# Optimization experiments

Hardware: AMD Instinct MI355X
Metric: run time of the kernel (lower is better)

Reference implementation:

```python
import jax, jax.numpy as jnp
import numpy as np

F = 256  # features
B, N = 16, 2048


def setup_inputs() -> dict:
    key = jax.random.key(0)
    ks = jax.random.split(key, 12)
    s = 1.0 / np.sqrt(F)
    return {
        "x": jax.random.normal(ks[0], (B, N, F), dtype=jnp.float32),
        "p": jax.random.normal(ks[1], (B, N, 3), dtype=jnp.float32),
        # nn.Linear weights: [out, in], y = x @ W.T + b
        "Wq": jax.random.normal(ks[2], (F, F), dtype=jnp.float32) * s,
        "bq": jax.random.normal(ks[3], (F,), dtype=jnp.float32) * s,
        "Wk": jax.random.normal(ks[4], (F, F), dtype=jnp.float32) * s,
        "bk": jax.random.normal(ks[5], (F,), dtype=jnp.float32) * s,
        "Wv": jax.random.normal(ks[6], (F, F), dtype=jnp.float32) * s,
        "bv": jax.random.normal(ks[7], (F,), dtype=jnp.float32) * s,
        # Conv1d kernel_size=1 == pointwise linear: W1 [F,3], W2 [F,F]
        "W1": jax.random.normal(ks[8], (F, 3), dtype=jnp.float32) * (1.0 / np.sqrt(3.0)),
        "b1": jax.random.normal(ks[9], (F,), dtype=jnp.float32) * (1.0 / np.sqrt(3.0)),
        "W2": jax.random.normal(ks[10], (F, F), dtype=jnp.float32) * s,
        "b2": jax.random.normal(ks[11], (F,), dtype=jnp.float32) * s,
    }


def reference(x, p, Wq, bq, Wk, bk, Wv, bv, W1, b1, W2, b2):
    # Positional encoder: Conv1d(3->F, k=1) + ReLU + Conv1d(F->F, k=1)
    pos = jnp.maximum(p @ W1.T + b1, 0.0) @ W2.T + b2  # [B, N, F]
    h = x + pos
    # NOTE: the original code swaps names: x_query = self.key(x), x_key = self.query(x)
    q = h @ Wk.T + bk  # x_query
    k = h @ Wq.T + bq  # x_key
    v = h @ Wv.T + bv  # x_value
    scale = 1.0 / np.sqrt(float(F))
    scores = jnp.einsum("bnf,bmf->bnm", q, k) * scale  # [B, N, N]
    attn = jax.nn.softmax(scores, axis=-1)
    return jnp.einsum("bnm,bmf->bnf", attn, v)  # [B, N, F]
```

## Files before the change

kernel.cpp:

```cpp
#include <hip/hip_runtime.h>

#define FEAT 256
#define SEQ  2048
#define NBATCH 16

typedef float  f32x4  __attribute__((ext_vector_type(4)));
typedef __bf16 bf16x8 __attribute__((ext_vector_type(8)));

__device__ __forceinline__ unsigned short f2bf(float f) {
  union { float f; unsigned int u; } v; v.f = f;
  unsigned int r = (v.u + 0x7fffu + ((v.u >> 16) & 1u)) >> 16;
  return (unsigned short)r;
}
__device__ __forceinline__ float bf2f(unsigned short u) {
  union { unsigned int u; float f; } v; v.u = ((unsigned int)u) << 16;
  return v.f;
}
__device__ __forceinline__ unsigned int pack2bf(float a, float b) {
  return (unsigned int)f2bf(a) | ((unsigned int)f2bf(b) << 16);
}

__device__ __forceinline__ float redsum16(float t) {
  t += __shfl_xor(t, 1);
  t += __shfl_xor(t, 2);
  t += __shfl_xor(t, 4);
  t += __shfl_xor(t, 8);
  return t;
}

__global__ __launch_bounds__(256) void k_wcvt(
    const float* __restrict__ Wq, const float* __restrict__ Wk,
    const float* __restrict__ Wv, const float* __restrict__ W2,
    unsigned short* __restrict__ Wqb, unsigned short* __restrict__ Wkb,
    unsigned short* __restrict__ Wvb, unsigned short* __restrict__ W2b) {
  int i = blockIdx.x * 256 + threadIdx.x;
  Wqb[i] = f2bf(Wq[i]);
  Wkb[i] = f2bf(Wk[i]);
  Wvb[i] = f2bf(Wv[i]);
  W2b[i] = f2bf(W2[i]);
}

__global__ __launch_bounds__(256) void k_pos_h(
    const float* __restrict__ x, const float* __restrict__ p,
    const float* __restrict__ W1, const float* __restrict__ b1,
    const unsigned short* __restrict__ W2b, const float* __restrict__ b2,
    unsigned short* __restrict__ hb) {
  __shared__ __align__(16) unsigned short tlds[64 * 264];
  __shared__ float pl[192];
  const int tid = threadIdx.x;
  const int blk = blockIdx.x;
  const int tok0 = blk * 64;
  if (tid < 192) pl[tid] = p[tok0 * 3 + tid];
  __syncthreads();
  const int j = tid;
  const float w0 = W1[j * 3 + 0], w1 = W1[j * 3 + 1], w2 = W1[j * 3 + 2];
  const float bb = b1[j];
#pragma unroll 4
  for (int tl = 0; tl < 64; ++tl) {
    float v = bb + pl[tl * 3 + 0] * w0 + pl[tl * 3 + 1] * w1 + pl[tl * 3 + 2] * w2;
    v = v > 0.f ? v : 0.f;
    tlds[tl * 264 + j] = f2bf(v);
  }
  __syncthreads();
  const int w = tid >> 6, lane = tid & 63;
  const int col = lane & 15, quad = lane >> 4;
  bf16x8 af[8];
  const unsigned short* arow = tlds + (w * 16 + col) * 264 + quad * 8;
#pragma unroll
  for (int ks = 0; ks < 8; ++ks) af[ks] = *(const bf16x8*)(arow + ks * 32);
#pragma unroll 1
  for (int ct = 0; ct < 16; ++ct) {
    f32x4 acc = {0.f, 0.f, 0.f, 0.f};
    const unsigned short* brow = W2b + (ct * 16 + col) * 256 + quad * 8;
#pragma unroll
    for (int ks = 0; ks < 8; ++ks) {
      bf16x8 bf = *(const bf16x8*)(brow + ks * 32);
      acc = __builtin_amdgcn_mfma_f32_16x16x32_bf16(af[ks], bf, acc, 0, 0, 0);
    }
    const int f = ct * 16 + col;
    const float bias = b2[f];
#pragma unroll
    for (int r = 0; r < 4; ++r) {
      const int tok = tok0 + w * 16 + quad * 4 + r;
      float v = acc[r] + bias + x[tok * 256 + f];
      hb[tok * 256 + f] = f2bf(v);
    }
  }
}

__global__ __launch_bounds__(256) void k_qkv(
    const unsigned short* __restrict__ hb,
    const unsigned short* __restrict__ Wqb, const float* __restrict__ bq,
    const unsigned short* __restrict__ Wkb, const float* __restrict__ bk,
    const unsigned short* __restrict__ Wvb, const float* __restrict__ bv,
    unsigned short* __restrict__ qb, unsigned short* __restrict__ kb,
    unsigned short* __restrict__ vtb) {
  const int tid = threadIdx.x, blk = blockIdx.x;
  const int ct0 = blockIdx.y * 8;
  const int w = tid >> 6, lane = tid & 63;
  const int col = lane & 15, quad = lane >> 4;
  const int row0 = blk * 128 + w * 32;
  bf16x8 af0[8], af1[8];
  const unsigned short* arow0 = hb + (size_t)(row0 + col) * 256 + quad * 8;
  const unsigned short* arow1 = arow0 + 16 * 256;
#pragma unroll
  for (int ks = 0; ks < 8; ++ks) {
    af0[ks] = *(const bf16x8*)(arow0 + ks * 32);
    af1[ks] = *(const bf16x8*)(arow1 + ks * 32);
  }
#pragma unroll 1
  for (int mat = 0; mat < 3; ++mat) {
    const unsigned short* W = (mat == 0) ? Wkb : ((mat == 1) ? Wqb : Wvb);
    const float* bias = (mat == 0) ? bk : ((mat == 1) ? bq : bv);
#pragma unroll 1
    for (int ct = ct0; ct < ct0 + 8; ++ct) {
      f32x4 a0 = {0.f, 0.f, 0.f, 0.f}, a1 = {0.f, 0.f, 0.f, 0.f};
      const unsigned short* brow = W + (ct * 16 + col) * 256 + quad * 8;
#pragma unroll
      for (int ks = 0; ks < 8; ++ks) {
        bf16x8 bf = *(const bf16x8*)(brow + ks * 32);
        a0 = __builtin_amdgcn_mfma_f32_16x16x32_bf16(af0[ks], bf, a0, 0, 0, 0);
        a1 = __builtin_amdgcn_mfma_f32_16x16x32_bf16(af1[ks], bf, a1, 0, 0, 0);
      }
      const int f = ct * 16 + col;
      const float bs = bias[f];
      if (mat < 2) {
        unsigned short* dst = (mat == 0) ? qb : kb;
#pragma unroll
        for (int r = 0; r < 4; ++r) {
          dst[(size_t)(row0 + quad * 4 + r) * 256 + f] = f2bf(a0[r] + bs);
          dst[(size_t)(row0 + 16 + quad * 4 + r) * 256 + f] = f2bf(a1[r] + bs);
        }
      } else {
        uint4 pk;
        pk.x = pack2bf(a0[0] + bs, a1[0] + bs);
        pk.y = pack2bf(a0[1] + bs, a1[1] + bs);
        pk.z = pack2bf(a0[2] + bs, a1[2] + bs);
        pk.w = pack2bf(a0[3] + bs, a1[3] + bs);
        const int t0 = row0 + quad * 4;
        const int b0 = t0 >> 11, n = t0 & 2047;
        const int g = n >> 5, ki = n & 31;
        *(uint4*)(vtb + (size_t)(b0 * 256 + f) * 2048 + g * 32 + 2 * ki) = pk;
      }
    }
  }
}

__global__ __launch_bounds__(256, 2) void k_attn(
    const unsigned short* __restrict__ qb, const unsigned short* __restrict__ kb,
    const unsigned short* __restrict__ vtb, float* __restrict__ outA,
    unsigned short* __restrict__ obB, float* __restrict__ lbuf) {
  __shared__ __align__(16) unsigned short Kl[32 * 264];
  __shared__ __align__(16) unsigned short Vt[256 * 40];
  __shared__ __align__(16) unsigned short Pl[4][32 * 40];
  const int tid = threadIdx.x;
  const int bx = blockIdx.x, b = blockIdx.y, h = blockIdx.z;
  const int w = tid >> 6, lane = tid & 63;
  const int col = lane & 15, quad = lane >> 4;
  const int n0 = bx * 128 + w * 32;
  const float scale = 0.0625f;

  bf16x8 qf0[8], qf1[8];
  const unsigned short* qrow0 = qb + (size_t)(b * 2048 + n0 + col) * 256 + quad * 8;
  const unsigned short* qrow1 = qrow0 + 16 * 256;
#pragma unroll
  for (int ks = 0; ks < 8; ++ks) {
    qf0[ks] = *(const bf16x8*)(qrow0 + ks * 32);
    qf1[ks] = *(const bf16x8*)(qrow1 + ks * 32);
  }

  f32x4 O0[16], O1[16];
#pragma unroll
  for (int ft = 0; ft < 16; ++ft) {
    O0[ft] = (f32x4){0.f, 0.f, 0.f, 0.f};
    O1[ft] = (f32x4){0.f, 0.f, 0.f, 0.f};
  }
  float ls0[4], ls1[4];
#pragma unroll
  for (int r = 0; r < 4; ++r) { ls0[r] = 0.f; ls1[r] = 0.f; }

  const uint4* ksrc = (const uint4*)(kb) + (size_t)b * 2048 * 32;
  const uint4* vsrc = (const uint4*)(vtb);
  unsigned short* Pw = Pl[w];
  const int kt0 = h * 32;

  for (int kt2 = 0; kt2 < 32; ++kt2) {
    const int kt = kt0 + kt2;
    __syncthreads();
    {
#pragma unroll
      for (int pp = 0; pp < 4; ++pp) {
        const int idx = pp * 256 + tid;
        const int r = idx >> 5, c = idx & 31;
        *(uint4*)(Kl + r * 264 + c * 8) = ksrc[(size_t)(kt * 32 + r) * 32 + c];
        const int f = idx >> 2, cc = idx & 3;
        *(uint4*)(Vt + f * 40 + cc * 8) =
            vsrc[(size_t)(b * 256 + f) * 256 + kt * 4 + cc];
      }
    }
    __syncthreads();
    f32x4 s00 = {0.f, 0.f, 0.f, 0.f}, s01 = {0.f, 0.f, 0.f, 0.f};
    f32x4 s10 = {0.f, 0.f, 0.f, 0.f}, s11 = {0.f, 0.f, 0.f, 0.f};
#pragma unroll
    for (int ks = 0; ks < 8; ++ks) {
      bf16x8 k0 = *(const bf16x8*)(Kl + col * 264 + ks * 32 + quad * 8);
      bf16x8 k1 = *(const bf16x8*)(Kl + (16 + col) * 264 + ks * 32 + quad * 8);
      s00 = __builtin_amdgcn_mfma_f32_16x16x32_bf16(qf0[ks], k0, s00, 0, 0, 0);
      s01 = __builtin_amdgcn_mfma_f32_16x16x32_bf16(qf0[ks], k1, s01, 0, 0, 0);
      s10 = __builtin_amdgcn_mfma_f32_16x16x32_bf16(qf1[ks], k0, s10, 0, 0, 0);
      s11 = __builtin_amdgcn_mfma_f32_16x16x32_bf16(qf1[ks], k1, s11, 0, 0, 0);
    }
#pragma unroll
    for (int r = 0; r < 4; ++r) {
      float p0 = __expf(fmaf(s00[r], scale, -8.0f));
      float p1 = __expf(fmaf(s01[r], scale, -8.0f));
      ls0[r] += p0 + p1;
      *(unsigned int*)(Pw + (quad * 4 + r) * 40 + 2 * col) = pack2bf(p0, p1);
      float q0 = __expf(fmaf(s10[r], scale, -8.0f));
      float q1 = __expf(fmaf(s11[r], scale, -8.0f));
      ls1[r] += q0 + q1;
      *(unsigned int*)(Pw + (16 + quad * 4 + r) * 40 + 2 * col) = pack2bf(q0, q1);
    }
    bf16x8 pf0 = *(const bf16x8*)(Pw + col * 40 + quad * 8);
    bf16x8 pf1 = *(const bf16x8*)(Pw + (16 + col) * 40 + quad * 8);
#pragma unroll
    for (int ft = 0; ft < 16; ++ft) {
      bf16x8 vf = *(const bf16x8*)(Vt + (ft * 16 + col) * 40 + quad * 8);
      O0[ft] = __builtin_amdgcn_mfma_f32_16x16x32_bf16(pf0, vf, O0[ft], 0, 0, 0);
      O1[ft] = __builtin_amdgcn_mfma_f32_16x16x32_bf16(pf1, vf, O1[ft], 0, 0, 0);
    }
  }
  float sr0[4], sr1[4];
#pragma unroll
  for (int r = 0; r < 4; ++r) {
    sr0[r] = redsum16(ls0[r]);
    sr1[r] = redsum16(ls1[r]);
  }
  if (h == 0) {
    if (col == 0) {
#pragma unroll
      for (int r = 0; r < 4; ++r) {
        lbuf[b * 2048 + n0 + quad * 4 + r] = sr0[r];
        lbuf[b * 2048 + n0 + 16 + quad * 4 + r] = sr1[r];
      }
    }
#pragma unroll
    for (int ft = 0; ft < 16; ++ft) {
#pragma unroll
      for (int r = 0; r < 4; ++r) {
        const int n = n0 + quad * 4 + r;
        outA[(size_t)(b * 2048 + n) * 256 + ft * 16 + col] = O0[ft][r];
        outA[(size_t)(b * 2048 + n + 16) * 256 + ft * 16 + col] = O1[ft][r];
      }
    }
  } else {
    if (col == 0) {
#pragma unroll
      for (int r = 0; r < 4; ++r) {
        lbuf[32768 + b * 2048 + n0 + quad * 4 + r] = sr0[r];
        lbuf[32768 + b * 2048 + n0 + 16 + quad * 4 + r] = sr1[r];
      }
    }
#pragma unroll
    for (int ft = 0; ft < 16; ++ft) {
#pragma unroll
      for (int r = 0; r < 4; ++r) {
        const int n = n0 + quad * 4 + r;
        obB[(size_t)(b * 2048 + n) * 256 + ft * 16 + col] = f2bf(O0[ft][r]);
        obB[(size_t)(b * 2048 + n + 16) * 256 + ft * 16 + col] = f2bf(O1[ft][r]);
      }
    }
  }
}

__global__ __launch_bounds__(256) void k_reduce(
    float* __restrict__ out, const unsigned short* __restrict__ ob,
    const float* __restrict__ lbuf) {
  const size_t i4 = (size_t)blockIdx.x * 256 + threadIdx.x;
  const int bn = (int)(i4 >> 6);
  const float rl = 1.0f / (lbuf[bn] + lbuf[32768 + bn]);
  float4 o = ((const float4*)out)[i4];
  ushort4 b4 = ((const ushort4*)ob)[i4];
  o.x = (o.x + bf2f(b4.x)) * rl;
  o.y = (o.y + bf2f(b4.y)) * rl;
  o.z = (o.z + bf2f(b4.z)) * rl;
  o.w = (o.w + bf2f(b4.w)) * rl;
  ((float4*)out)[i4] = o;
}

extern "C" void kernel_launch(void* const* d_in, const int* in_sizes, int n_in,
                              void* d_out, int out_size, void* d_ws, size_t ws_size,
                              hipStream_t stream) {
  const float* x  = (const float*)d_in[0];
  const float* p  = (const float*)d_in[1];
  const float* Wq = (const float*)d_in[2];
  const float* bq = (const float*)d_in[3];
  const float* Wk = (const float*)d_in[4];
  const float* bk = (const float*)d_in[5];
  const float* Wv = (const float*)d_in[6];
  const float* bv = (const float*)d_in[7];
  const float* W1 = (const float*)d_in[8];
  const float* b1 = (const float*)d_in[9];
  const float* W2 = (const float*)d_in[10];
  const float* b2 = (const float*)d_in[11];
  float* out = (float*)d_out;

  char* ws = (char*)d_ws;
  unsigned short* W2b = (unsigned short*)(ws + 0);
  unsigned short* Wqb = (unsigned short*)(ws + 131072);
  unsigned short* Wkb = (unsigned short*)(ws + 262144);
  unsigned short* Wvb = (unsigned short*)(ws + 393216);
  unsigned short* hb  = (unsigned short*)(ws + 524288);
  unsigned short* qb  = (unsigned short*)(ws + 524288 + 16777216);
  unsigned short* kb  = (unsigned short*)(ws + 524288 + 2 * 16777216);
  unsigned short* vtb = (unsigned short*)(ws + 524288 + 3 * 16777216);
  float* lbuf = (float*)(ws + 524288 + 4 * 16777216);

  k_wcvt<<<256, 256, 0, stream>>>(Wq, Wk, Wv, W2, Wqb, Wkb, Wvb, W2b);
  k_pos_h<<<512, 256, 0, stream>>>(x, p, W1, b1, W2b, b2, hb);
  k_qkv<<<dim3(256, 2), 256, 0, stream>>>(hb, Wqb, bq, Wkb, bk, Wvb, bv, qb, kb, vtb);
  k_attn<<<dim3(16, 16, 2), 256, 0, stream>>>(qb, kb, vtb, out, hb, lbuf);
  k_reduce<<<8192, 256, 0, stream>>>(out, hb, lbuf);
}
```

Measured before the change: 327.9 us.

## Double-buffer K/V tiles with direct global-to-LDS loads and tile-contiguous layouts

The projection kernel now writes K and V^T in a tile-blocked global layout, so each 32-key tile is one contiguous 16 KB chunk already in the order MFMA fragments need. The attention kernel streams these tiles with global_load_lds straight into two ping-pong LDS buffers, prefetching tile kt+1 while computing on tile kt. This removes the register round-trip and one of the two barriers per iteration, and overlaps global latency with compute. In exchange LDS per block roughly doubles, which could limit occupancy. Correctness also depends on the compiler waiting on the async LDS loads before the barrier.

```diff
diff --git a/kernel.cpp b/kernel.cpp
--- a/kernel.cpp
+++ b/kernel.cpp
@@ -26,6 +26,12 @@
   t += __shfl_xor(t, 4);
   t += __shfl_xor(t, 8);
   return t;
+}
+
+__device__ __forceinline__ void gld16(const unsigned short* g, unsigned short* l) {
+  __builtin_amdgcn_global_load_lds(
+      (const __attribute__((address_space(1))) unsigned int*)(const void*)g,
+      (__attribute__((address_space(3))) unsigned int*)(void*)l, 16, 0, 0);
 }
 
 __global__ __launch_bounds__(256) void k_wcvt(
@@ -124,12 +130,23 @@
       }
       const int f = ct * 16 + col;
       const float bs = bias[f];
-      if (mat < 2) {
-        unsigned short* dst = (mat == 0) ? qb : kb;
+      if (mat == 0) {
 #pragma unroll
         for (int r = 0; r < 4; ++r) {
-          dst[(size_t)(row0 + quad * 4 + r) * 256 + f] = f2bf(a0[r] + bs);
-          dst[(size_t)(row0 + 16 + quad * 4 + r) * 256 + f] = f2bf(a1[r] + bs);
+          qb[(size_t)(row0 + quad * 4 + r) * 256 + f] = f2bf(a0[r] + bs);
+          qb[(size_t)(row0 + 16 + quad * 4 + r) * 256 + f] = f2bf(a1[r] + bs);
+        }
+      } else if (mat == 1) {
+        const int ks_ = f >> 5, qk = (f >> 3) & 3, jj = f & 7;
+#pragma unroll
+        for (int r = 0; r < 4; ++r) {
+          const int tok = row0 + quad * 4 + r;
+          const int b0 = tok >> 11, n = tok & 2047;
+          const int g = n >> 5, key = n & 31;
+          const size_t base =
+              ((((size_t)(b0 * 64 + g) * 8 + ks_) * 4 + qk) * 32);
+          kb[(base + key) * 8 + jj] = f2bf(a0[r] + bs);
+          kb[(base + key + 16) * 8 + jj] = f2bf(a1[r] + bs);
         }
       } else {
         uint4 pk;
@@ -139,8 +156,8 @@
         pk.w = pack2bf(a0[3] + bs, a1[3] + bs);
         const int t0 = row0 + quad * 4;
         const int b0 = t0 >> 11, n = t0 & 2047;
-        const int g = n >> 5, ki = n & 31;
-        *(uint4*)(vtb + (size_t)(b0 * 256 + f) * 2048 + g * 32 + 2 * ki) = pk;
+        const int g = n >> 5;
+        *(uint4*)(vtb + (((size_t)(b0 * 64 + g) * 4 + quad) * 256 + f) * 8) = pk;
       }
     }
   }
@@ -150,8 +167,8 @@
     const unsigned short* __restrict__ qb, const unsigned short* __restrict__ kb,
     const unsigned short* __restrict__ vtb, float* __restrict__ outA,
     unsigned short* __restrict__ obB, float* __restrict__ lbuf) {
-  __shared__ __align__(16) unsigned short Kl[32 * 264];
-  __shared__ __align__(16) unsigned short Vt[256 * 40];
+  __shared__ __align__(16) unsigned short Kl[2][8192];
+  __shared__ __align__(16) unsigned short Vt[2][8192];
   __shared__ __align__(16) unsigned short Pl[4][32 * 40];
   const int tid = threadIdx.x;
   const int bx = blockIdx.x, b = blockIdx.y, h = blockIdx.z;
@@ -179,32 +196,38 @@
 #pragma unroll
   for (int r = 0; r < 4; ++r) { ls0[r] = 0.f; ls1[r] = 0.f; }
 
-  const uint4* ksrc = (const uint4*)(kb) + (size_t)b * 2048 * 32;
-  const uint4* vsrc = (const uint4*)(vtb);
+  const unsigned short* kbase = kb + (size_t)b * 64 * 8192;
+  const unsigned short* vbase = vtb + (size_t)b * 64 * 8192;
   unsigned short* Pw = Pl[w];
   const int kt0 = h * 32;
+  const int sl = w * 2048 + lane * 8;
+
+#pragma unroll
+  for (int q = 0; q < 4; ++q) {
+    gld16(kbase + (size_t)kt0 * 8192 + sl + q * 512, &Kl[0][sl + q * 512]);
+    gld16(vbase + (size_t)kt0 * 8192 + sl + q * 512, &Vt[0][sl + q * 512]);
+  }
 
   for (int kt2 = 0; kt2 < 32; ++kt2) {
-    const int kt = kt0 + kt2;
+    const int cur = kt2 & 1;
+    const unsigned short* Kc = Kl[cur];
+    const unsigned short* Vc = Vt[cur];
     __syncthreads();
-    {
-#pragma unroll
-      for (int pp = 0; pp < 4; ++pp) {
-        const int idx = pp * 256 + tid;
-        const int r = idx >> 5, c = idx & 31;
-        *(uint4*)(Kl + r * 264 + c * 8) = ksrc[(size_t)(kt * 32 + r) * 32 + c];
-        const int f = idx >> 2, cc = idx & 3;
-        *(uint4*)(Vt + f * 40 + cc * 8) =
-            vsrc[(size_t)(b * 256 + f) * 256 + kt * 4 + cc];
-      }
-    }
-    __syncthreads();
+    if (kt2 + 1 < 32) {
+      const size_t tb = (size_t)(kt0 + kt2 + 1) * 8192;
+#pragma unroll
+      for (int q = 0; q < 4; ++q) {
+        gld16(kbase + tb + sl + q * 512, &Kl[cur ^ 1][sl + q * 512]);
+        gld16(vbase + tb + sl + q * 512, &Vt[cur ^ 1][sl + q * 512]);
+      }
+    }
     f32x4 s00 = {0.f, 0.f, 0.f, 0.f}, s01 = {0.f, 0.f, 0.f, 0.f};
     f32x4 s10 = {0.f, 0.f, 0.f, 0.f}, s11 = {0.f, 0.f, 0.f, 0.f};
 #pragma unroll
     for (int ks = 0; ks < 8; ++ks) {
-      bf16x8 k0 = *(const bf16x8*)(Kl + col * 264 + ks * 32 + quad * 8);
-      bf16x8 k1 = *(const bf16x8*)(Kl + (16 + col) * 264 + ks * 32 + quad * 8);
+      const unsigned short* kc = Kc + (ks * 4 + quad) * 256 + col * 8;
+      bf16x8 k0 = *(const bf16x8*)(kc);
+      bf16x8 k1 = *(const bf16x8*)(kc + 128);
       s00 = __builtin_amdgcn_mfma_f32_16x16x32_bf16(qf0[ks], k0, s00, 0, 0, 0);
       s01 = __builtin_amdgcn_mfma_f32_16x16x32_bf16(qf0[ks], k1, s01, 0, 0, 0);
       s10 = __builtin_amdgcn_mfma_f32_16x16x32_bf16(qf1[ks], k0, s10, 0, 0, 0);
@@ -225,7 +248,7 @@
     bf16x8 pf1 = *(const bf16x8*)(Pw + (16 + col) * 40 + quad * 8);
 #pragma unroll
     for (int ft = 0; ft < 16; ++ft) {
-      bf16x8 vf = *(const bf16x8*)(Vt + (ft * 16 + col) * 40 + quad * 8);
+      bf16x8 vf = *(const bf16x8*)(Vc + quad * 2048 + (ft * 16 + col) * 8);
       O0[ft] = __builtin_amdgcn_mfma_f32_16x16x32_bf16(pf0, vf, O0[ft], 0, 0, 0);
       O1[ft] = __builtin_amdgcn_mfma_f32_16x16x32_bf16(pf1, vf, O1[ft], 0, 0, 0);
     }
```

Result: faster. 279.2 us (-14.8%).
